# Optimization experiments

Measured on AMD Instinct MI355X. Metric: run time of the kernel, lower is better.

The kernel has to match this reference:

```python
import jax, jax.numpy as jnp
import numpy as np

N, T, D, H = 100000, 16, 8, 40
HP1 = H + 1
ALPHA_DP = 1.0
KAPPA0 = 1000.0   # priorGaussianVarKappa
NU0 = 100.0       # priorWishartNu
PSI0_SCALE = 500.0  # priorWishartPsi = 500*I


def setup_inputs() -> dict:
    key = jax.random.key(0)
    ks = jax.random.split(key, 6)
    return {
        "BetaGamma1": jnp.ones((1, T), jnp.float32),
        "Phi": jax.random.uniform(ks[0], (N, T), jnp.float32),
        "inputData": jax.random.normal(ks[1], (N, D), jnp.float32),
        "outputData": jax.random.normal(ks[2], (N, 1), jnp.float32),
        "weightELM": jax.random.uniform(ks[3], (D, H), jnp.float32) * 2.0 - 1.0,
        "biasELM": jax.random.normal(ks[4], (H, 1), jnp.float32),
        "epsilonA": jnp.ones((1, T), jnp.float32),
        "epsilonB": jnp.ones((1, T), jnp.float32),
        "zetaA": 1e-4 * jnp.ones((1, T), jnp.float32),
        "zetaB": jnp.ones((1, T), jnp.float32),
    }


def reference(BetaGamma1, Phi, inputData, outputData, weightELM, biasELM,
              epsilonA, epsilonB, zetaA, zetaB):
    f32 = jnp.float32
    mu0 = jnp.zeros((D, 1), f32)                      # priorGaussianMeanMu
    Psi0 = PSI0_SCALE * jnp.eye(D, dtype=f32)         # priorWishartPsi

    sumPhi = jnp.sum(Phi, axis=0, keepdims=True)      # [1,T]

    # stick-breaking Beta params. Torch builds a flipped [T,N,T] tril mask;
    # mathematically BetaGamma2[t] = alpha + sum_{j>t} sum_n Phi[n,j]
    BetaGamma1_new = jnp.ones_like(BetaGamma1) + sumPhi
    col = sumPhi[0]                                   # [T]
    rev_incl = jnp.cumsum(col[::-1])[::-1]            # sum_{j>=t}
    BetaGamma2 = (ALPHA_DP + (rev_incl - col))[None, :]

    # Gaussian-Wishart natural-parameter updates.
    # Torch loops over clusters doing [N,D,D] bmm outer products; this is
    # S[:,:,t] = sum_n Phi[n,t] x_n x_n^T
    S = jnp.einsum('nt,ni,nj->ijt', Phi, inputData, inputData)  # [D,D,T]
    t11 = -0.5 * (Psi0 + KAPPA0 * mu0 @ mu0.T)[:, :, None] - 0.5 * S
    t12 = KAPPA0 * mu0 + inputData.T @ Phi            # [D,T]
    t21 = -0.5 * sumPhi - 0.5 * (NU0 + D + 2)         # [1,T]
    kappa = KAPPA0 + sumPhi                           # [1,T]
    mu = t12 / kappa                                  # [D,T]
    nu = -2.0 * t21 - 2.0 - float(D)                  # [1,T]
    psi = -2.0 * t11 - kappa[0][None, None, :] * jnp.einsum('it,jt->ijt', mu, mu)

    # ELM feature map + augmented design matrix X = [sigmoid(x W + b), 1]
    hmap = jax.nn.sigmoid(inputData @ weightELM + biasELM.T)   # [N,H]
    X = jnp.concatenate([hmap, jnp.ones((inputData.shape[0], 1), f32)], axis=1)  # [N,HP1]

    epsExp = (epsilonA / epsilonB)[0]                 # [T]
    zetaExp = (zetaA / zetaB)[0]                      # [T]

    # A[t] = X^T diag(Phi[:,t]) X   (torch: per-cluster bmm with diag_embed)
    A = jnp.einsum('nt,ni,nj->tij', Phi, X, X)        # [T,HP1,HP1]
    WS = jnp.linalg.inv(epsExp[:, None, None] * A
                        + zetaExp[:, None, None] * jnp.eye(HP1, dtype=f32))
    # b[t] = X^T diag(Phi[:,t]) y
    b = jnp.einsum('ni,nt->ti', X * outputData, Phi)  # [T,HP1]
    WMv = zetaExp[:, None] * jnp.einsum('tij,tj->ti', WS, b)   # [T,HP1]
    WM = WMv[:, :, None]                              # [T,HP1,1]

    # prior Zeta/Epsilon alias the variational initial values in __init__
    zetaA_new = zetaA + (H + 1) * 0.5
    zetaB_new = zetaB + 0.5 * (jnp.sum(WMv * WMv, axis=1)
                               + jnp.trace(WS, axis1=-2, axis2=-1))[None, :]
    epsA_new = epsilonA + 0.5 * sumPhi

    pred = jnp.einsum('ni,ti->tn', X, WMv)            # [T,N]
    err = outputData.T - pred                          # [T,N]
    t1 = jnp.einsum('tn,nt->t', err * err, Phi)[None, :]
    t2 = jnp.einsum('tij,tji->t', A, WS)[None, :]
    epsB_new = epsilonB + 0.5 * (t1 + t2)

    return (BetaGamma1_new, BetaGamma2, mu, kappa, nu, psi,
            WM, WS, zetaA_new, zetaB_new, epsA_new, epsB_new)
```

## Files before the change

kernel.cpp:

```cpp
#include <hip/hip_runtime.h>

#define Nn 100000
#define Tt 16
#define Dd 8
#define Hh 40
#define HP1 41

#define SPC 8
#define CH  (32 * SPC)
#define KCMAX ((Nn + CH - 1) / CH)

#define NPAIR 1275
#define PSZ (NPAIR * 16)

#define XEH_OFF  0
#define XEL_OFF  (XEH_OFF + 32 * Nn)
#define PHIT_OFF (XEL_OFF + 32 * Nn)
#define PART_OFF (PHIT_OFF + 16 * Nn)
#define P_OFF    (PART_OFF + 8 * PSZ)

#define OFF_BG1   0
#define OFF_BG2   16
#define OFF_MU    32
#define OFF_KAPPA 160
#define OFF_NU    176
#define OFF_PSI   192
#define OFF_WM    1216
#define OFF_WS    1872
#define OFF_ZA    28768
#define OFF_ZB    28784
#define OFF_EA    28800
#define OFF_EB    28816

typedef _Float16 f16x8 __attribute__((ext_vector_type(8)));
typedef float f32x4 __attribute__((ext_vector_type(4)));
typedef unsigned int u32x4 __attribute__((ext_vector_type(4)));

__device__ __forceinline__ int pidx(int i, int j) {
  if (i > j) { int tmp = i; i = j; j = tmp; }
  return (i * (2 * 50 - i + 1)) / 2 + (j - i);
}

__global__ __launch_bounds__(256)
void elm_expand(const float* __restrict__ Phi, const float* __restrict__ Xd,
                const float* __restrict__ Yd, const float* __restrict__ W,
                const float* __restrict__ bb,
                unsigned short* __restrict__ XeHi, unsigned short* __restrict__ XeLo,
                float* __restrict__ PhiT)
{
  __shared__ float sW[Dd * Hh];
  __shared__ float sb[Hh];
  __shared__ float xs[64][9];
  __shared__ float ys[64];
  __shared__ float hrow[64][41];
  __shared__ float pt[16][68];
  int tid = threadIdx.x;
  int n0 = blockIdx.x * 64;

  for (int i = tid; i < Dd * Hh; i += 256) sW[i] = W[i];
  if (tid < Hh) sb[tid] = bb[tid];
  if (tid < 128) {
    int nl = tid >> 1, h4 = (tid & 1) * 4;
    int gn = n0 + nl;
    float4 v = (gn < Nn) ? *(const float4*)(Xd + (size_t)gn * 8 + h4)
                         : make_float4(0.f, 0.f, 0.f, 0.f);
    xs[nl][h4 + 0] = v.x; xs[nl][h4 + 1] = v.y;
    xs[nl][h4 + 2] = v.z; xs[nl][h4 + 3] = v.w;
  }
  if (tid < 64) { int gn = n0 + tid; ys[tid] = (gn < Nn) ? Yd[gn] : 0.f; }
  {
    int nl = tid >> 2, q = tid & 3;
    int gn = n0 + nl;
    float4 v = (gn < Nn) ? *(const float4*)(Phi + (size_t)gn * 16 + q * 4)
                         : make_float4(0.f, 0.f, 0.f, 0.f);
    pt[q * 4 + 0][nl] = v.x; pt[q * 4 + 1][nl] = v.y;
    pt[q * 4 + 2][nl] = v.z; pt[q * 4 + 3][nl] = v.w;
  }
  __syncthreads();
  {
    int nl = tid >> 2, hq = (tid & 3) * 10;
    for (int hh = 0; hh < 10; ++hh) {
      int h = hq + hh;
      float z = sb[h];
#pragma unroll
      for (int d = 0; d < 8; ++d) z = fmaf(xs[nl][d], sW[d * Hh + h], z);
      hrow[nl][h] = 1.f / (1.f + __expf(-z));
    }
  }
  __syncthreads();
  {
    int t = tid & 15, nq = tid >> 4;
    int gn = n0 + nq * 4;
    if (gn < Nn) {
      float4 v = make_float4(pt[t][nq * 4 + 0], pt[t][nq * 4 + 1],
                             pt[t][nq * 4 + 2], pt[t][nq * 4 + 3]);
      *(float4*)(PhiT + (size_t)t * Nn + gn) = v;
    }
  }
  {
    int cidx = tid >> 2, seg = tid & 3;
    int nl0 = seg * 16;
    float vv[16];
#pragma unroll
    for (int j = 0; j < 16; ++j) {
      int n = nl0 + j;
      float v;
      if (cidx < Hh) v = hrow[n][cidx];
      else if (cidx == 40) v = 1.f;
      else if (cidx < 49) v = xs[n][cidx - 41];
      else if (cidx == 49) v = ys[n];
      else v = 0.f;
      vv[j] = v;
    }
    unsigned short hs[16], ls[16];
#pragma unroll
    for (int j = 0; j < 16; ++j) {
      _Float16 h = (_Float16)vv[j];
      float r = vv[j] - (float)h;
      _Float16 lo = (_Float16)r;
      hs[j] = __builtin_bit_cast(unsigned short, h);
      ls[j] = __builtin_bit_cast(unsigned short, lo);
    }
#pragma unroll
    for (int q2 = 0; q2 < 2; ++q2) {
      int gn = n0 + nl0 + q2 * 8;
      if (gn < Nn) {
        uint4 uh, ul;
        uh.x = hs[q2*8+0] | ((unsigned)hs[q2*8+1] << 16);
        uh.y = hs[q2*8+2] | ((unsigned)hs[q2*8+3] << 16);
        uh.z = hs[q2*8+4] | ((unsigned)hs[q2*8+5] << 16);
        uh.w = hs[q2*8+6] | ((unsigned)hs[q2*8+7] << 16);
        ul.x = ls[q2*8+0] | ((unsigned)ls[q2*8+1] << 16);
        ul.y = ls[q2*8+2] | ((unsigned)ls[q2*8+3] << 16);
        ul.z = ls[q2*8+4] | ((unsigned)ls[q2*8+5] << 16);
        ul.w = ls[q2*8+6] | ((unsigned)ls[q2*8+7] << 16);
        *(uint4*)(XeHi + (size_t)cidx * Nn + gn) = uh;
        *(uint4*)(XeLo + (size_t)cidx * Nn + gn) = ul;
      }
    }
  }
}

__device__ __forceinline__ void gload16(const void* g, void* l) {
  __builtin_amdgcn_global_load_lds(
      (const __attribute__((address_space(1))) unsigned int*)g,
      (__attribute__((address_space(3))) unsigned int*)l, 16, 0, 0);
}

#define PHI_LDS 32768
#define LDS_BYTES (PHI_LDS + 16 * CH * 4)

__global__ __launch_bounds__(512, 2)
void gram_mfma(const float* __restrict__ PhiT,
               const unsigned short* __restrict__ XeHi,
               const unsigned short* __restrict__ XeLo,
               float* __restrict__ P)
{
  __shared__ __align__(16) char smem[LDS_BYTES];

  int tid = threadIdx.x;
  int l = tid & 63, w = tid >> 6;
  int l15 = l & 15, lg = l >> 4;

  int MT  = (w < 4) ? 7 : 6;
  int i0w = (w < 4) ? 7 * w : 28 + 6 * (w - 4);

  int off_b[4];
#pragma unroll
  for (int nt = 0; nt < 4; ++nt) {
    int j = l15 + 16 * nt;
    off_b[nt] = j * 64 + 16 * (lg ^ (j & 3));
  }
  int off_a[7];
#pragma unroll
  for (int mi = 0; mi < 7; ++mi) {
    int i = i0w + mi;
    off_a[mi] = i * 64 + 16 * (lg ^ (i & 3));
  }
  int off_p0 = l15 * 128 + 16 * ((2 * lg) ^ (l15 & 7));
  int off_p1 = l15 * 128 + 16 * ((2 * lg + 1) ^ (l15 & 7));
  int ld0 = tid * 16;
  int brow = (tid & 255) >> 2, bsl = tid & 3;
  const unsigned short* bplane = (tid < 256) ? XeHi : XeLo;

  f32x4 acc[7][4];
#pragma unroll
  for (int mi = 0; mi < 7; ++mi)
#pragma unroll
    for (int nt = 0; nt < 4; ++nt) acc[mi][nt] = (f32x4){0.f, 0.f, 0.f, 0.f};

  for (int cc = blockIdx.x; cc < KCMAX; cc += gridDim.x) {
    int n0 = cc * CH;
    int rem = Nn - n0; if (rem > CH) rem = CH;
    int nsteps = rem >> 5;

    __builtin_amdgcn_s_barrier();
    asm volatile("" ::: "memory");

    const char* gB = (const char*)(bplane + (size_t)brow * Nn + n0
                                   + 8 * (bsl ^ (brow & 3)));
#define STAGE(sx) gload16(gB + (size_t)(sx) * 64, \
                          &smem[(((sx) & 3) * 8192) + ld0])

#pragma unroll
    for (int q = 0; q < 2; ++q) {
      int gp = tid + q * 512;
      int s = gp >> 7, qq = gp & 127, t = qq >> 3, sl = qq & 7;
      gload16(PhiT + (size_t)t * Nn + n0 + s * 32 + 4 * (sl ^ (t & 7)),
              &smem[PHI_LDS + gp * 16]);
    }
    STAGE(0);
    if (nsteps > 1) STAGE(1);
    if (nsteps > 2) STAGE(2);

    for (int s = 0; s < nsteps; ++s) {
      int out = nsteps - 1 - s; if (out > 2) out = 2;
      if (out == 2)      asm volatile("s_waitcnt vmcnt(2)" ::: "memory");
      else if (out == 1) asm volatile("s_waitcnt vmcnt(1)" ::: "memory");
      else               asm volatile("s_waitcnt vmcnt(0)" ::: "memory");
      __builtin_amdgcn_s_barrier();
      asm volatile("" ::: "memory");
      if (s + 3 < nsteps) STAGE(s + 3);

      const char* base  = &smem[(s & 3) * 8192];
      const char* pbase = &smem[PHI_LDS + s * 2048];
      f32x4 p0 = *(const f32x4*)(pbase + off_p0);
      f32x4 p1 = *(const f32x4*)(pbase + off_p1);
      float ph[8] = {p0[0], p0[1], p0[2], p0[3], p1[0], p1[1], p1[2], p1[3]};

      f16x8 bh[4], bl[4];
#pragma unroll
      for (int nt = 0; nt < 4; ++nt) {
        bh[nt] = *(const f16x8*)(base + off_b[nt]);
        bl[nt] = *(const f16x8*)(base + 4096 + off_b[nt]);
      }
      __builtin_amdgcn_s_setprio(1);
#pragma unroll
      for (int mi = 0; mi < 7; ++mi) {
        if (mi >= MT) break;
        f16x8 xh = *(const f16x8*)(base + off_a[mi]);
        f16x8 xl = *(const f16x8*)(base + 4096 + off_a[mi]);
        float v0 = ph[0] * ((float)xh[0] + (float)xl[0]);
        float v1 = ph[1] * ((float)xh[1] + (float)xl[1]);
        float v2 = ph[2] * ((float)xh[2] + (float)xl[2]);
        float v3 = ph[3] * ((float)xh[3] + (float)xl[3]);
        float v4 = ph[4] * ((float)xh[4] + (float)xl[4]);
        float v5 = ph[5] * ((float)xh[5] + (float)xl[5]);
        float v6 = ph[6] * ((float)xh[6] + (float)xl[6]);
        float v7 = ph[7] * ((float)xh[7] + (float)xl[7]);
        auto h0 = __builtin_amdgcn_cvt_pkrtz(v0, v1);
        auto h1 = __builtin_amdgcn_cvt_pkrtz(v2, v3);
        auto h2 = __builtin_amdgcn_cvt_pkrtz(v4, v5);
        auto h3 = __builtin_amdgcn_cvt_pkrtz(v6, v7);
        float r0 = v0 - (float)h0[0], r1 = v1 - (float)h0[1];
        float r2 = v2 - (float)h1[0], r3 = v3 - (float)h1[1];
        float r4 = v4 - (float)h2[0], r5 = v5 - (float)h2[1];
        float r6 = v6 - (float)h3[0], r7 = v7 - (float)h3[1];
        auto e0 = __builtin_amdgcn_cvt_pkrtz(r0, r1);
        auto e1 = __builtin_amdgcn_cvt_pkrtz(r2, r3);
        auto e2 = __builtin_amdgcn_cvt_pkrtz(r4, r5);
        auto e3 = __builtin_amdgcn_cvt_pkrtz(r6, r7);
        u32x4 uh = {__builtin_bit_cast(unsigned int, h0), __builtin_bit_cast(unsigned int, h1),
                    __builtin_bit_cast(unsigned int, h2), __builtin_bit_cast(unsigned int, h3)};
        u32x4 ul = {__builtin_bit_cast(unsigned int, e0), __builtin_bit_cast(unsigned int, e1),
                    __builtin_bit_cast(unsigned int, e2), __builtin_bit_cast(unsigned int, e3)};
        f16x8 ah = __builtin_bit_cast(f16x8, uh);
        f16x8 al = __builtin_bit_cast(f16x8, ul);
#pragma unroll
        for (int nt = 0; nt < 4; ++nt) {
          acc[mi][nt] = __builtin_amdgcn_mfma_f32_16x16x32_f16(ah, bh[nt], acc[mi][nt], 0, 0, 0);
          acc[mi][nt] = __builtin_amdgcn_mfma_f32_16x16x32_f16(ah, bl[nt], acc[mi][nt], 0, 0, 0);
          acc[mi][nt] = __builtin_amdgcn_mfma_f32_16x16x32_f16(al, bh[nt], acc[mi][nt], 0, 0, 0);
        }
      }
      __builtin_amdgcn_s_setprio(0);
    }
#undef STAGE
  }

  float* Pc = P + (size_t)blockIdx.x * PSZ;
#pragma unroll
  for (int mi = 0; mi < 7; ++mi) {
    if (mi >= MT) break;
    int i = i0w + mi;
    if (i < 50) {
#pragma unroll
      for (int nt = 0; nt < 4; ++nt) {
        int j = nt * 16 + l15;
        if (j >= i && j < 50) {
          int pb = (i * (101 - i)) / 2 + (j - i);
          *(f32x4*)(Pc + pb * 16 + lg * 4) = acc[mi][nt];
        }
      }
    }
  }
}

__global__ __launch_bounds__(256)
void reduce_a(const float4* __restrict__ P4, int nslabs, float4* __restrict__ part4)
{
  int g = blockIdx.y;
  int idx = blockIdx.x * 256 + threadIdx.x;
  if (idx >= PSZ / 4) return;
  int per = (nslabs + 7) / 8;
  int c0 = g * per, c1 = c0 + per; if (c1 > nslabs) c1 = nslabs;
  float4 s = make_float4(0.f, 0.f, 0.f, 0.f);
  for (int cc = c0; cc < c1; ++cc) {
    float4 v = P4[(size_t)cc * (PSZ / 4) + idx];
    s.x += v.x; s.y += v.y; s.z += v.z; s.w += v.w;
  }
  part4[(size_t)g * (PSZ / 4) + idx] = s;
}

__device__ __forceinline__ float accv(const float* __restrict__ part, int idx) {
  float s = 0.f;
#pragma unroll
  for (int g = 0; g < 8; ++g) s += part[g * PSZ + idx];
  return s;
}

__global__ __launch_bounds__(256)
void finalize_kernel(const float* __restrict__ part, const float* __restrict__ epsA,
                     const float* __restrict__ epsB, const float* __restrict__ zetA,
                     const float* __restrict__ zetB, float* __restrict__ out)
{
  int t = blockIdx.x;
  int tid = threadIdx.x;
  __shared__ float G[HP1][84];
  __shared__ float As[HP1][HP1 + 1];
  __shared__ float bs[HP1];
  __shared__ float colk[HP1];
  __shared__ float red[256];
  __shared__ float wmv[HP1];
  __shared__ float rowv[4][HP1 + 1];
  __shared__ float mus[Dd];

  float epsExp = epsA[t] / epsB[t];
  float zetaExp = zetA[t] / zetB[t];

  for (int idx = tid; idx < HP1 * HP1; idx += 256) {
    int i = idx / HP1, j = idx % HP1;
    float a = accv(part, pidx(i, j) * Tt + t);
    As[i][j] = a;
    G[i][j] = epsExp * a + (i == j ? zetaExp : 0.f);
    G[i][41 + j] = (i == j) ? 1.f : 0.f;
  }
  for (int idx = tid; idx < HP1; idx += 256) {
    G[idx][82] = 0.f; G[idx][83] = 0.f;
    bs[idx] = accv(part, pidx(idx, 49) * Tt + t);
  }
  __syncthreads();

  int c = tid % HP1;
  int ig = tid / HP1;
  int irow0 = ig * 7;

  for (int k = 0; k < HP1; ++k) {
    float pivinv = 1.f / G[k][k];
    if (tid >= 1 && tid <= HP1) G[k][k + tid] *= pivinv;
    if (tid < HP1) colk[tid] = (tid == k) ? 0.f : G[tid][k];
    __syncthreads();
    if (ig < 6) {
      int j = k + 1 + c;
      float pk = G[k][j];
#pragma unroll
      for (int r = 0; r < 7; ++r) {
        int i = irow0 + r;
        if (i < HP1 && i != k) G[i][j] = fmaf(-colk[i], pk, G[i][j]);
      }
    }
    __syncthreads();
  }

  for (int idx = tid; idx < HP1 * HP1; idx += 256) {
    int i = idx / HP1, j = idx % HP1;
    out[OFF_WS + (t * HP1 + i) * HP1 + j] = G[i][41 + j];
  }
  if (tid < HP1) {
    float s = 0.f;
    for (int j = 0; j < HP1; ++j) s += G[tid][41 + j] * bs[j];
    float w = zetaExp * s;
    wmv[tid] = w;
    out[OFF_WM + t * HP1 + tid] = w;
  }
  __syncthreads();
  float lt2 = 0.f;
  for (int idx = tid; idx < HP1 * HP1; idx += 256) {
    int i = idx / HP1, j = idx % HP1;
    lt2 += As[i][j] * G[i][41 + j];
  }
  red[tid] = lt2; __syncthreads();
  for (int s = 128; s > 0; s >>= 1) {
    if (tid < s) red[tid] += red[tid + s];
    __syncthreads();
  }
  float t2v = red[0];
  if (tid < HP1) {
    float w = wmv[tid];
    float aw = 0.f;
    for (int j = 0; j < HP1; ++j) aw += As[tid][j] * wmv[j];
    rowv[0][tid] = w * bs[tid];
    rowv[1][tid] = w * w;
    rowv[2][tid] = G[tid][41 + tid];
    rowv[3][tid] = w * aw;
  }
  __syncthreads();

  float sp = accv(part, pidx(40, 40) * Tt + t);
  float kap = 1000.f + sp;
  float syy = accv(part, pidx(49, 49) * Tt + t);

  if (tid == 0) {
    float wb = 0.f, wn = 0.f, trc = 0.f, quad = 0.f;
    for (int i = 0; i < HP1; ++i) {
      wb += rowv[0][i]; wn += rowv[1][i]; trc += rowv[2][i]; quad += rowv[3][i];
    }
    float t1 = syy - 2.f * wb + quad;
    out[OFF_BG1 + t] = 1.f + sp;
    float rest = 0.f;
    for (int u = t + 1; u < Tt; ++u) rest += accv(part, pidx(40, 40) * Tt + u);
    out[OFF_BG2 + t] = 1.f + rest;
    out[OFF_KAPPA + t] = kap;
    out[OFF_NU + t] = sp + 100.f;
    out[OFF_ZA + t] = zetA[t] + 0.5f * (float)HP1;
    out[OFF_ZB + t] = zetB[t] + 0.5f * (wn + trc);
    out[OFF_EA + t] = epsA[t] + 0.5f * sp;
    out[OFF_EB + t] = epsB[t] + 0.5f * (t1 + t2v);
  }
  if (tid < Dd) {
    float m = accv(part, pidx(40, 41 + tid) * Tt + t) / kap;
    mus[tid] = m;
    out[OFF_MU + tid * Tt + t] = m;
  }
  __syncthreads();
  if (tid < Dd * Dd) {
    int i = tid / Dd, j = tid % Dd;
    float S = accv(part, pidx(41 + i, 41 + j) * Tt + t);
    float v = (i == j ? 500.f : 0.f) + S - kap * mus[i] * mus[j];
    out[OFF_PSI + (i * Dd + j) * Tt + t] = v;
  }
}

extern "C" void kernel_launch(void* const* d_in, const int* in_sizes, int n_in,
                              void* d_out, int out_size, void* d_ws, size_t ws_size,
                              hipStream_t stream) {
  const float* Phi = (const float*)d_in[1];
  const float* Xd  = (const float*)d_in[2];
  const float* Yd  = (const float*)d_in[3];
  const float* W   = (const float*)d_in[4];
  const float* bb  = (const float*)d_in[5];
  const float* eA  = (const float*)d_in[6];
  const float* eB  = (const float*)d_in[7];
  const float* zA  = (const float*)d_in[8];
  const float* zB  = (const float*)d_in[9];
  float* out = (float*)d_out;
  float* ws  = (float*)d_ws;

  unsigned short* XeHi = (unsigned short*)(ws + XEH_OFF);
  unsigned short* XeLo = (unsigned short*)(ws + XEL_OFF);
  float* PhiT = ws + PHIT_OFF;
  float* part = ws + PART_OFF;
  float* P    = ws + P_OFF;

  long maxSlabs = ((long)(ws_size / 4) - (long)P_OFF) / PSZ;
  int grid1 = (int)(maxSlabs < KCMAX ? maxSlabs : KCMAX);
  if (grid1 < 1) grid1 = 1;

  hipLaunchKernelGGL(elm_expand, dim3((Nn + 63) / 64), dim3(256), 0, stream,
                     Phi, Xd, Yd, W, bb, XeHi, XeLo, PhiT);
  hipLaunchKernelGGL(gram_mfma, dim3(grid1), dim3(512), 0, stream,
                     PhiT, XeHi, XeLo, P);
  hipLaunchKernelGGL(reduce_a, dim3(20, 8), dim3(256), 0, stream,
                     (const float4*)P, grid1, (float4*)part);
  hipLaunchKernelGGL(finalize_kernel, dim3(Tt), dim3(256), 0, stream,
                     part, eA, eB, zA, zB, out);
}
```

Before: 188.0 us.

## Split gram MFMA kernel into four M-slice blocks of 256 threads per chunk group

The gram kernel now uses 256-thread blocks and four blocks per N-chunk group, each covering 13 rows of the 50-row output instead of one 512-thread block covering all rows. Each thread stages both hi and lo planes, the LDS swizzle changes to use (row>>1)&3, and Phi loads are clamped at the tail. The aim is more concurrent blocks and better occupancy (launch bounds 256,3) with fewer accumulators per thread. The cost is that each chunk's X and Phi data is loaded four times, once per M-slice block. Whether a block's partial result lands in its own slab depends on rows not overlapping across blocks, and the code seems to rely on that.

After: 183.9 us. 1.02x faster.

```diff
diff --git a/kernel.cpp b/kernel.cpp
--- a/kernel.cpp
+++ b/kernel.cpp
@@ -150,46 +150,48 @@
 #define PHI_LDS 32768
 #define LDS_BYTES (PHI_LDS + 16 * CH * 4)
 
-__global__ __launch_bounds__(512, 2)
+__global__ __launch_bounds__(256, 3)
 void gram_mfma(const float* __restrict__ PhiT,
                const unsigned short* __restrict__ XeHi,
                const unsigned short* __restrict__ XeLo,
-               float* __restrict__ P)
+               float* __restrict__ P, int G)
 {
   __shared__ __align__(16) char smem[LDS_BYTES];
 
   int tid = threadIdx.x;
   int l = tid & 63, w = tid >> 6;
   int l15 = l & 15, lg = l >> 4;
-
-  int MT  = (w < 4) ? 7 : 6;
-  int i0w = (w < 4) ? 7 * w : 28 + 6 * (w - 4);
+  int bM = blockIdx.x & 3, g = blockIdx.x >> 2;
+  int i0 = bM * 13;
+
+  int mbase = (w == 0) ? 0 : (1 + 3 * w);
+  int MT = (w == 0) ? 4 : 3;
 
   int off_b[4];
 #pragma unroll
   for (int nt = 0; nt < 4; ++nt) {
     int j = l15 + 16 * nt;
-    off_b[nt] = j * 64 + 16 * (lg ^ (j & 3));
-  }
-  int off_a[7];
-#pragma unroll
-  for (int mi = 0; mi < 7; ++mi) {
-    int i = i0w + mi;
-    off_a[mi] = i * 64 + 16 * (lg ^ (i & 3));
-  }
-  int off_p0 = l15 * 128 + 16 * ((2 * lg) ^ (l15 & 7));
-  int off_p1 = l15 * 128 + 16 * ((2 * lg + 1) ^ (l15 & 7));
-  int ld0 = tid * 16;
-  int brow = (tid & 255) >> 2, bsl = tid & 3;
-  const unsigned short* bplane = (tid < 256) ? XeHi : XeLo;
-
-  f32x4 acc[7][4];
-#pragma unroll
-  for (int mi = 0; mi < 7; ++mi)
+    off_b[nt] = j * 64 + 16 * (lg ^ ((j >> 1) & 3));
+  }
+  int off_a[4];
+#pragma unroll
+  for (int mi = 0; mi < 4; ++mi) {
+    int i = i0 + mbase + mi;
+    off_a[mi] = i * 64 + 16 * (lg ^ ((i >> 1) & 3));
+  }
+  int off_p0 = PHI_LDS + l15 * 128 + 16 * ((2 * lg) ^ (l15 & 7));
+  int off_p1 = PHI_LDS + l15 * 128 + 16 * ((2 * lg + 1) ^ (l15 & 7));
+
+  int srow = tid >> 2;
+  int ssl = (tid & 3) ^ ((srow >> 1) & 3);
+
+  f32x4 acc[4][4];
+#pragma unroll
+  for (int mi = 0; mi < 4; ++mi)
 #pragma unroll
     for (int nt = 0; nt < 4; ++nt) acc[mi][nt] = (f32x4){0.f, 0.f, 0.f, 0.f};
 
-  for (int cc = blockIdx.x; cc < KCMAX; cc += gridDim.x) {
+  for (int cc = g; cc < KCMAX; cc += G) {
     int n0 = cc * CH;
     int rem = Nn - n0; if (rem > CH) rem = CH;
     int nsteps = rem >> 5;
@@ -197,16 +199,21 @@
     __builtin_amdgcn_s_barrier();
     asm volatile("" ::: "memory");
 
-    const char* gB = (const char*)(bplane + (size_t)brow * Nn + n0
-                                   + 8 * (bsl ^ (brow & 3)));
-#define STAGE(sx) gload16(gB + (size_t)(sx) * 64, \
-                          &smem[(((sx) & 3) * 8192) + ld0])
-
-#pragma unroll
-    for (int q = 0; q < 2; ++q) {
-      int gp = tid + q * 512;
-      int s = gp >> 7, qq = gp & 127, t = qq >> 3, sl = qq & 7;
-      gload16(PhiT + (size_t)t * Nn + n0 + s * 32 + 4 * (sl ^ (t & 7)),
+    const char* gH = (const char*)(XeHi + (size_t)srow * Nn + n0 + 8 * ssl);
+    const char* gL = (const char*)(XeLo + (size_t)srow * Nn + n0 + 8 * ssl);
+#define STAGE(sx) do {                                                    \
+    gload16(gH + (size_t)(sx) * 64, &smem[(((sx) & 3) * 8192) + tid * 16]);\
+    gload16(gL + (size_t)(sx) * 64,                                       \
+            &smem[(((sx) & 3) * 8192) + 4096 + tid * 16]);                \
+  } while (0)
+
+#pragma unroll
+    for (int q = 0; q < 4; ++q) {
+      int gp = tid + q * 256;
+      int s = gp >> 7, t = (gp & 127) >> 3, sl = gp & 7;
+      int nsrc = n0 + s * 32;
+      if (nsrc > Nn - 32) nsrc = Nn - 32;
+      gload16(PhiT + (size_t)t * Nn + nsrc + 4 * (sl ^ (t & 7)),
               &smem[PHI_LDS + gp * 16]);
     }
     STAGE(0);
@@ -215,15 +222,15 @@
 
     for (int s = 0; s < nsteps; ++s) {
       int out = nsteps - 1 - s; if (out > 2) out = 2;
-      if (out == 2)      asm volatile("s_waitcnt vmcnt(2)" ::: "memory");
-      else if (out == 1) asm volatile("s_waitcnt vmcnt(1)" ::: "memory");
+      if (out == 2)      asm volatile("s_waitcnt vmcnt(4)" ::: "memory");
+      else if (out == 1) asm volatile("s_waitcnt vmcnt(2)" ::: "memory");
       else               asm volatile("s_waitcnt vmcnt(0)" ::: "memory");
       __builtin_amdgcn_s_barrier();
       asm volatile("" ::: "memory");
       if (s + 3 < nsteps) STAGE(s + 3);
 
       const char* base  = &smem[(s & 3) * 8192];
-      const char* pbase = &smem[PHI_LDS + s * 2048];
+      const char* pbase = &smem[s * 2048];
       f32x4 p0 = *(const f32x4*)(pbase + off_p0);
       f32x4 p1 = *(const f32x4*)(pbase + off_p1);
       float ph[8] = {p0[0], p0[1], p0[2], p0[3], p1[0], p1[1], p1[2], p1[3]};
@@ -236,7 +243,7 @@
       }
       __builtin_amdgcn_s_setprio(1);
 #pragma unroll
-      for (int mi = 0; mi < 7; ++mi) {
+      for (int mi = 0; mi < 4; ++mi) {
         if (mi >= MT) break;
         f16x8 xh = *(const f16x8*)(base + off_a[mi]);
         f16x8 xl = *(const f16x8*)(base + 4096 + off_a[mi]);
@@ -278,11 +285,11 @@
 #undef STAGE
   }
 
-  float* Pc = P + (size_t)blockIdx.x * PSZ;
-#pragma unroll
-  for (int mi = 0; mi < 7; ++mi) {
+  float* Pc = P + (size_t)g * PSZ;
+#pragma unroll
+  for (int mi = 0; mi < 4; ++mi) {
     if (mi >= MT) break;
-    int i = i0w + mi;
+    int i = i0 + mbase + mi;
     if (i < 50) {
 #pragma unroll
       for (int nt = 0; nt < 4; ++nt) {
@@ -463,15 +470,15 @@
   float* P    = ws + P_OFF;
 
   long maxSlabs = ((long)(ws_size / 4) - (long)P_OFF) / PSZ;
-  int grid1 = (int)(maxSlabs < KCMAX ? maxSlabs : KCMAX);
-  if (grid1 < 1) grid1 = 1;
+  int G = (int)(maxSlabs < KCMAX ? maxSlabs : KCMAX);
+  if (G < 1) G = 1;
 
   hipLaunchKernelGGL(elm_expand, dim3((Nn + 63) / 64), dim3(256), 0, stream,
                      Phi, Xd, Yd, W, bb, XeHi, XeLo, PhiT);
-  hipLaunchKernelGGL(gram_mfma, dim3(grid1), dim3(512), 0, stream,
-                     PhiT, XeHi, XeLo, P);
+  hipLaunchKernelGGL(gram_mfma, dim3(4 * G), dim3(256), 0, stream,
+                     PhiT, XeHi, XeLo, P, G);
   hipLaunchKernelGGL(reduce_a, dim3(20, 8), dim3(256), 0, stream,
-                     (const float4*)P, grid1, (float4*)part);
+                     (const float4*)P, G, (float4*)part);
   hipLaunchKernelGGL(finalize_kernel, dim3(Tt), dim3(256), 0, stream,
                      part, eA, eB, zA, zB, out);
 }
```
